# Kernel optimization log

Hardware: AMD Instinct MI355X
Metric: run time of the kernel (lower is better)

Reference implementation:

```python
import jax, jax.numpy as jnp
import numpy as np

USR_NUM = 100000
D_IN = 32
D_HID = 32
D_MID = 16
D_OUT = 2
N_EDGES = 1600000
EPS = 1e-16  # matches torch_geometric.utils.softmax denominator eps


def _glorot(key, shape):
    fan_in, fan_out = shape[0], shape[1]
    lim = np.sqrt(6.0 / (fan_in + fan_out))
    return jax.random.uniform(key, shape, jnp.float32, -lim, lim)


def setup_inputs() -> dict:
    key = jax.random.key(0)
    ks = jax.random.split(key, 16)
    inp = {
        "edge_index": jax.random.randint(ks[0], (2, N_EDGES), 0, USR_NUM, dtype=jnp.int64)
        if jax.config.jax_enable_x64 else jax.random.randint(ks[0], (2, N_EDGES), 0, USR_NUM).astype(jnp.int32),
        "emb": jax.random.normal(ks[1], (USR_NUM, D_IN), jnp.float32),
        # conv1: TransformerConv(32 -> 32, heads=1)
        "Wq1": _glorot(ks[2], (D_IN, D_HID)), "bq1": jnp.zeros((D_HID,), jnp.float32),
        "Wk1": _glorot(ks[3], (D_IN, D_HID)), "bk1": jnp.zeros((D_HID,), jnp.float32),
        "Wv1": _glorot(ks[4], (D_IN, D_HID)), "bv1": jnp.zeros((D_HID,), jnp.float32),
        "Ws1": _glorot(ks[5], (D_IN, D_HID)), "bs1": jnp.zeros((D_HID,), jnp.float32),
        # conv2: TransformerConv(32 -> 16, heads=1)
        "Wq2": _glorot(ks[6], (D_HID, D_MID)), "bq2": jnp.zeros((D_MID,), jnp.float32),
        "Wk2": _glorot(ks[7], (D_HID, D_MID)), "bk2": jnp.zeros((D_MID,), jnp.float32),
        "Wv2": _glorot(ks[8], (D_HID, D_MID)), "bv2": jnp.zeros((D_MID,), jnp.float32),
        "Ws2": _glorot(ks[9], (D_HID, D_MID)), "bs2": jnp.zeros((D_MID,), jnp.float32),
        # output: Linear(16 -> 2)
        "Wo": _glorot(ks[10], (D_MID, D_OUT)), "bo": jnp.zeros((D_OUT,), jnp.float32),
    }
    return inp


def transformer_conv(x, src, dst, Wq, bq, Wk, bk, Wv, bv, Ws, bs, n_nodes):
    # edge (j=src -> i=dst): alpha_ij = softmax_i( <q_i, k_j> / sqrt(d) )
    d = Wq.shape[1]
    q = (x @ Wq + bq)[dst]          # [E, d]
    k = (x @ Wk + bk)[src]          # [E, d]
    v = (x @ Wv + bv)[src]          # [E, d]
    alpha = jnp.sum(q * k, axis=-1) / jnp.sqrt(jnp.float32(d))  # [E]
    # segment softmax over incoming edges of each destination node
    seg_max = jax.ops.segment_max(alpha, dst, num_segments=n_nodes)  # [N]
    e = jnp.exp(alpha - seg_max[dst])
    seg_sum = jax.ops.segment_sum(e, dst, num_segments=n_nodes)      # [N]
    w = e / (seg_sum[dst] + EPS)
    agg = jax.ops.segment_sum(v * w[:, None], dst, num_segments=n_nodes)  # [N, d]
    return agg + x @ Ws + bs  # root/skip connection (PyG default root_weight=True)


def reference(edge_index, emb,
              Wq1, bq1, Wk1, bk1, Wv1, bv1, Ws1, bs1,
              Wq2, bq2, Wk2, bk2, Wv2, bv2, Ws2, bs2,
              Wo, bo):
    src, dst = edge_index[0], edge_index[1]
    h = transformer_conv(emb, src, dst, Wq1, bq1, Wk1, bk1, Wv1, bv1, Ws1, bs1, USR_NUM)
    h = jax.nn.relu(h)
    h = transformer_conv(h, src, dst, Wq2, bq2, Wk2, bk2, Wv2, bv2, Ws2, bs2, USR_NUM)
    h = jax.nn.relu(h)
    return h @ Wo + bo  # [N, 2]
```

## Files before the change

### kernel.cpp

```cpp
#include <hip/hip_runtime.h>
#include <hip/hip_bf16.h>

typedef __hip_bfloat16 bf16;
typedef unsigned int uint;
typedef unsigned short ushort;

#define N_NODES 100000
#define N_EDGES_C 1600000
#define NSB2 392
#define NSB2P 512
#define RND 2048
#define EPB (RND / 256)
#define NBIN 64
#define G_RAD ((N_EDGES_C + RND - 1) / RND)
#define HCAP 5632
#define NSLOT (NSB2 * 256)
#define NCHUNK 8
#define KEYN (256 * NCHUNK)

__device__ __forceinline__ float ldf(const void* p, long i, int isbf) {
    return isbf ? __bfloat162float(((const bf16*)p)[i]) : ((const float*)p)[i];
}
__device__ __forceinline__ int ldidx(const int* ei, long pos, int is64) {
    return is64 ? ei[2 * pos] : ei[pos];
}
__device__ __forceinline__ ushort bfb(float x) {
    bf16 h = __float2bfloat16(x);
    return *(ushort*)&h;
}
__device__ __forceinline__ float bl(uint u) { return __uint_as_float(u << 16); }
__device__ __forceinline__ float bh(uint u) { return __uint_as_float(u & 0xFFFF0000u); }

__global__ void setup_kernel(
    const void* emb, const int* ei,
    const void* Wq1, const void* bq1, const void* Wk1, const void* bk1,
    const void* Wv1, const void* bv1, const void* Ws1, const void* bs1,
    const void* Wq2, const void* bq2, const void* Wk2, const void* bk2,
    const void* Wv2, const void* bv2, const void* Ws2, const void* bs2,
    const void* Wo, const void* bo,
    int* flags, float* wp1, float* bp1, float* wp2, float* bp2, float* woF,
    int* curSB) {
    __shared__ int sf0;
    int t = threadIdx.x;
    if (t < 64) {
        const bf16* pb = (const bf16*)emb;
        int bad = 0;
        for (int i = t; i < 256; i += 64) {
            float v = __bfloat162float(pb[i]);
            if (!(v > -1.0e6f && v < 1.0e6f)) bad++;
        }
        int nz = 0;
        for (int i = 2 * t + 1; i < 256; i += 128) nz += (ei[i] != 0) ? 1 : 0;
#pragma unroll
        for (int m = 32; m >= 1; m >>= 1) {
            bad += __shfl_xor(bad, m, 64);
            nz  += __shfl_xor(nz, m, 64);
        }
        if (t == 0) {
            int f0 = (bad <= 8) ? 1 : 0;
            flags[0] = f0;
            flags[1] = (nz == 0) ? 1 : 0;
            sf0 = f0;
        }
    }
    __syncthreads();
    int isbf = sf0;
    for (int i = t; i < 1024; i += 256) {
        wp1[i]        = ldf(Wq1, i, isbf);
        wp1[1024 + i] = ldf(Wk1, i, isbf);
        wp1[2048 + i] = ldf(Wv1, i, isbf);
        wp1[3072 + i] = ldf(Ws1, i, isbf);
    }
    for (int i = t; i < 512; i += 256) {
        wp2[i]        = ldf(Wq2, i, isbf);
        wp2[512 + i]  = ldf(Wk2, i, isbf);
        wp2[1024 + i] = ldf(Wv2, i, isbf);
        wp2[1536 + i] = ldf(Ws2, i, isbf);
    }
    if (t < 32) {
        bp1[t] = ldf(bq1, t, isbf); bp1[32 + t] = ldf(bk1, t, isbf);
        bp1[64 + t] = ldf(bv1, t, isbf); bp1[96 + t] = ldf(bs1, t, isbf);
        woF[t] = ldf(Wo, t, isbf);
    }
    if (t < 16) {
        bp2[t] = ldf(bq2, t, isbf); bp2[16 + t] = ldf(bk2, t, isbf);
        bp2[32 + t] = ldf(bv2, t, isbf); bp2[48 + t] = ldf(bs2, t, isbf);
    }
    if (t < 2) woF[32 + t] = ldf(bo, t, isbf);
    curSB[t] = 0; curSB[t + 256] = 0;
}

template <int DOUT, bool RUNTIME_DTYPE>
__device__ __forceinline__ void node_linear_body(
    const void* __restrict__ X, const float* __restrict__ wpack,
    const float* __restrict__ bpack, const int* __restrict__ flags,
    float* __restrict__ q, ushort* __restrict__ kvb, float* __restrict__ s,
    int bid, float* __restrict__ sW, float* __restrict__ sbias, float* __restrict__ sX) {
    const int TPN = DOUT / 4;
    const int NPB = 256 / TPN;
    const int W_ELEMS = 4 * 32 * DOUT;

    const float4* wp4 = (const float4*)wpack;
    float4* sW4 = (float4*)sW;
    for (int i = threadIdx.x; i < W_ELEMS / 4; i += 256) sW4[i] = wp4[i];
    if (threadIdx.x < 4 * DOUT) sbias[threadIdx.x] = bpack[threadIdx.x];
    const int base = bid * NPB * 32;
    bool useBf = RUNTIME_DTYPE && (flags[0] != 0);
    if (useBf) {
        for (int i = threadIdx.x; i < NPB * 32; i += 256) {
            int g = base + i;
            float xv = (g < N_NODES * 32) ? __bfloat162float(((const bf16*)X)[g]) : 0.0f;
            sX[(i >> 5) * 36 + (i & 31)] = xv;
        }
    } else {
        for (int i = threadIdx.x; i < NPB * 32; i += 256) {
            int g = base + i;
            sX[(i >> 5) * 36 + (i & 31)] = (g < N_NODES * 32) ? ((const float*)X)[g] : 0.0f;
        }
    }
    __syncthreads();

    int l = threadIdx.x / TPN;
    int c4 = (threadIdx.x % TPN) * 4;
    int n = bid * NPB + l;
    if (n >= N_NODES) return;

    float xr[32];
#pragma unroll
    for (int j = 0; j < 8; j++) {
        float4 t4 = *(const float4*)&sX[l * 36 + 4 * j];
        xr[4 * j] = t4.x; xr[4 * j + 1] = t4.y; xr[4 * j + 2] = t4.z; xr[4 * j + 3] = t4.w;
    }
    float acc[4][4];
#pragma unroll
    for (int m = 0; m < 4; m++)
#pragma unroll
        for (int j = 0; j < 4; j++) acc[m][j] = sbias[m * DOUT + c4 + j];

#pragma unroll
    for (int t = 0; t < 32; t++) {
#pragma unroll
        for (int m = 0; m < 4; m++) {
            float4 w = *(const float4*)&sW[(m * 32 + t) * DOUT + c4];
            acc[m][0] += xr[t] * w.x;
            acc[m][1] += xr[t] * w.y;
            acc[m][2] += xr[t] * w.z;
            acc[m][3] += xr[t] * w.w;
        }
    }
    size_t o = (size_t)n * DOUT + c4;
    *(float4*)&q[o] = make_float4(acc[0][0], acc[0][1], acc[0][2], acc[0][3]);
    *(float4*)&s[o] = make_float4(acc[3][0], acc[3][1], acc[3][2], acc[3][3]);
    size_t okv = (size_t)n * 2 * DOUT + c4;
    ushort4 kp = make_ushort4(bfb(acc[1][0]), bfb(acc[1][1]), bfb(acc[1][2]), bfb(acc[1][3]));
    ushort4 vp = make_ushort4(bfb(acc[2][0]), bfb(acc[2][1]), bfb(acc[2][2]), bfb(acc[2][3]));
    *(ushort4*)&kvb[okv]        = kp;
    *(ushort4*)&kvb[okv + DOUT] = vp;
}

struct RadixS {
    int cnt[NSB2P]; int excl[NSB2P]; int gbase[NSB2P]; int wsum[4];
    uint sVal[RND]; ushort sSb[RND];
};
struct LinS { float sW[4096]; float sbias[128]; float sX[32 * 36]; };
union alignas(16) FusedS { RadixS r; LinS l; };

__global__ void __launch_bounds__(256, 4) fused_ra_nl(
    const int* __restrict__ ei, const int* __restrict__ flags,
    int* __restrict__ curSB, uint* __restrict__ pairsSB,
    const void* __restrict__ X, const float* __restrict__ wpack,
    const float* __restrict__ bpack,
    float* __restrict__ q, ushort* __restrict__ kvb, float* __restrict__ s) {
    __shared__ FusedS u;
    if (blockIdx.x >= G_RAD) {
        node_linear_body<32, true>(X, wpack, bpack, flags, q, kvb, s,
                                   (int)blockIdx.x - G_RAD, u.l.sW, u.l.sbias, u.l.sX);
        return;
    }
    int* cnt = u.r.cnt; int* excl = u.r.excl; int* gbase = u.r.gbase;
    uint* sVal = u.r.sVal; ushort* sSb = u.r.sSb;
    const int is64 = flags[1];
    int t = threadIdx.x;
    cnt[t] = 0; cnt[t + 256] = 0;
    __syncthreads();
    long base = (long)blockIdx.x * RND;

    int mySb[EPB]; int myRank[EPB]; uint myPk[EPB];
#pragma unroll
    for (int r = 0; r < EPB; r++) {
        long e = base + r * 256 + t;
        mySb[r] = -1;
        if (e < N_EDGES_C) {
            int d = ldidx(ei, (long)N_EDGES_C + e, is64);
            int src = ldidx(ei, e, is64);
            int sb = d >> 8;
            myPk[r] = (uint)src | ((uint)(d & 255) << 17);
            myRank[r] = atomicAdd(&cnt[sb], 1);
            mySb[r] = sb;
        }
    }
    __syncthreads();
    int v0 = cnt[2 * t], v1 = cnt[2 * t + 1];
    int sum2 = v0 + v1;
    int lane6 = t & 63, wid6 = t >> 6;
    int x = sum2;
#pragma unroll
    for (int off = 1; off < 64; off <<= 1) {
        int u2 = __shfl_up(x, off, 64);
        if (lane6 >= off) x += u2;
    }
    if (lane6 == 63) u.r.wsum[wid6] = x;
    __syncthreads();
    int wbase = 0;
#pragma unroll
    for (int w = 0; w < 4; w++) if (w < wid6) wbase += u.r.wsum[w];
    int basex = wbase + x - sum2;
    excl[2 * t]     = basex;
    excl[2 * t + 1] = basex + v0;
    __syncthreads();
#pragma unroll
    for (int r = 0; r < EPB; r++) {
        if (mySb[r] >= 0) {
            int pos = excl[mySb[r]] + myRank[r];
            sVal[pos] = myPk[r];
            sSb[pos] = (ushort)mySb[r];
        }
    }
    for (int i = t; i < NSB2P; i += 256)
        gbase[i] = (cnt[i] > 0) ? atomicAdd(&curSB[i], cnt[i]) : 0;
    __syncthreads();
    int tot = excl[NSB2P - 1] + cnt[NSB2P - 1];
    for (int i = t; i < tot; i += 256) {
        int sb = sSb[i];
        int gp = gbase[sb] + (i - excl[sb]);
        if (gp < HCAP)
            pairsSB[(size_t)sb * HCAP + gp] = sVal[i];
    }
}

__global__ void __launch_bounds__(512, 2) radix_b(
    const int* __restrict__ curSB, const uint* __restrict__ pairsSB,
    int* __restrict__ esrc,
    int* __restrict__ rowbeg, int* __restrict__ rowend,
    int* __restrict__ perm) {
    __shared__ uint sP[HCAP];
    __shared__ int dcnt[KEYN];
    __shared__ int dexcl[KEYN];
    __shared__ int wsum[4];
    __shared__ int hbin[NBIN], hbase[NBIN], hcur[NBIN];
    int sbh = blockIdx.x;
    int t = threadIdx.x;
    int n = min(curSB[sbh], HCAP);
    for (int i = t; i < KEYN; i += 512) dcnt[i] = 0;
    if (t < NBIN) { hbin[t] = 0; hcur[t] = 0; }
    if (t < 256) perm[sbh * 256 + t] = -1;
    __syncthreads();
    const uint* srcp = pairsSB + (size_t)sbh * HCAP;
    for (int i = t; i < n; i += 512) {
        uint pk = srcp[i];
        sP[i] = pk;
        int key = (int)((pk >> 17) & 255) * NCHUNK + (int)((pk & 0x1FFFFu) >> 14);
        atomicAdd(&dcnt[key], 1);
    }
    __syncthreads();
    int v = 0, myExcl = 0;
    if (t < 256) {
        const int kb = t * NCHUNK;
        int sum = 0;
#pragma unroll
        for (int j = 0; j < NCHUNK; j++) sum += dcnt[kb + j];
        v = sum;
        int lane6 = t & 63, wid6 = t >> 6;
        int x = v;
#pragma unroll
        for (int off = 1; off < 64; off <<= 1) {
            int u2 = __shfl_up(x, off, 64);
            if (lane6 >= off) x += u2;
        }
        if (lane6 == 63) wsum[wid6] = x;
        myExcl = x - v;
    }
    __syncthreads();
    if (t < 256) {
        int wid6 = t >> 6;
        int wbase = 0;
#pragma unroll
        for (int w = 0; w < 4; w++) if (w < wid6) wbase += wsum[w];
        myExcl += wbase;
        const int kb = t * NCHUNK;
        int run = myExcl;
#pragma unroll
        for (int j = 0; j < NCHUNK; j++) { dexcl[kb + j] = run; run += dcnt[kb + j]; }
    }
    __syncthreads();
    const int EB = sbh * HCAP;
    int dst = sbh * 256 + t;
    int mybin = -1;
    if (t < 256 && dst < N_NODES) {
        rowbeg[dst] = EB + min(myExcl, HCAP);
        rowend[dst] = EB + min(myExcl + v, HCAP);
        mybin = min(v, NBIN - 1);
        atomicAdd(&hbin[mybin], 1);
    }
    __syncthreads();
    if (t < 64) {
        int hv = hbin[t];
        int sfx = hv;
#pragma unroll
        for (int off = 1; off < 64; off <<= 1) {
            int u2 = __shfl_down(sfx, off, 64);
            if (t + off < 64) sfx += u2;
        }
        hbase[t] = sfx - hv;
    }
    __syncthreads();
    if (t < 256 && dst < N_NODES) {
        int r = atomicAdd(&hcur[mybin], 1);
        perm[sbh * 256 + hbase[mybin] + r] = dst;
    }
    for (int i = t; i < n; i += 512) {
        uint pk = sP[i];
        int key = (int)((pk >> 17) & 255) * NCHUNK + (int)((pk & 0x1FFFFu) >> 14);
        int p2 = atomicAdd(&dexcl[key], 1);
        if (p2 < HCAP) esrc[EB + p2] = (int)(pk & 0x1FFFF);
    }
}

__global__ void gather_attn_l1(const int* __restrict__ perm,
                               const int* __restrict__ rowbeg, const int* __restrict__ rowend,
                               const int* __restrict__ esrc,
                               const float* __restrict__ q, const ushort* __restrict__ kvb,
                               const float* __restrict__ s,
                               const float* __restrict__ wp2,
                               const float* __restrict__ bp2,
                               float* __restrict__ q2o, ushort* __restrict__ kvb2o,
                               float* __restrict__ s2o) {
    const int D = 32;
    const int LPD = 4;
    const int G = 16;
    __shared__ float sW2[2048];
    __shared__ float sb2[64];
    __shared__ float sH[64 * 36];
    __shared__ int sDst[64];

    for (int i = threadIdx.x; i < 2048; i += 256) sW2[i] = wp2[i];
    if (threadIdx.x < 64) sb2[threadIdx.x] = bp2[threadIdx.x];

    int lane = threadIdx.x & 63;
    int wave = (blockIdx.x * blockDim.x + threadIdx.x) >> 6;
    int g = lane / LPD;
    int c = lane % LPD;
    int idx = wave * G + g;
    int dst = perm[idx];
    bool alive = (dst >= 0);

    const float rsq = 0.17677669529663689f;
    float4 qa = make_float4(0.f, 0.f, 0.f, 0.f), qb = qa;
    int beg = 0, end = 0;
    if (alive) {
        qa = *(const float4*)(q + (size_t)dst * D + 8 * c);
        qb = *(const float4*)(q + (size_t)dst * D + 8 * c + 4);
        beg = rowbeg[dst]; end = rowend[dst];
    }

    const char* kvbase = (const char*)kvb;
    const int ROW = 4 * D;
    const int koff = 16 * c;
    const int voff = 2 * D + 16 * c;

    float sum0 = 0.f, sum1 = 0.f;
    float a0[8] = {0,0,0,0,0,0,0,0};
    float a1[8] = {0,0,0,0,0,0,0,0};

    uint4 kq[4], vq[4];
#pragma unroll
    for (int r = 0; r < 4; r++) {
        int sn = (beg + r < end) ? esrc[beg + r] : 0;
        const char* p = kvbase + (size_t)sn * ROW;
        kq[r] = *(const uint4*)(p + koff);
        vq[r] = *(const uint4*)(p + voff);
    }

    for (int e = beg; e < end; e += 4) {
        uint4 kc[4], vc[4];
#pragma unroll
        for (int r = 0; r < 4; r++) { kc[r] = kq[r]; vc[r] = vq[r]; }
#pragma unroll
        for (int r = 0; r < 4; r++) {
            if (e + 4 + r < end) {
                const char* p = kvbase + (size_t)esrc[e + 4 + r] * ROW;
                kq[r] = *(const uint4*)(p + koff);
                vq[r] = *(const uint4*)(p + voff);
            }
        }
#pragma unroll
        for (int r = 0; r < 4; r++) {
            if (e + r < end) {
                uint4 kA = kc[r], vA = vc[r];
                float pd = qa.x * bl(kA.x) + qa.y * bh(kA.x) + qa.z * bl(kA.y) + qa.w * bh(kA.y)
                         + qb.x * bl(kA.z) + qb.y * bh(kA.z) + qb.z * bl(kA.w) + qb.w * bh(kA.w);
#pragma unroll
                for (int m = LPD / 2; m >= 1; m >>= 1) pd += __shfl_xor(pd, m, LPD);
                float ex = __expf(fminf(fmaxf(pd * rsq, -80.0f), 80.0f));
                if (r & 1) {
                    sum1 += ex;
                    a1[0] += bl(vA.x) * ex; a1[1] += bh(vA.x) * ex;
                    a1[2] += bl(vA.y) * ex; a1[3] += bh(vA.y) * ex;
                    a1[4] += bl(vA.z) * ex; a1[5] += bh(vA.z) * ex;
                    a1[6] += bl(vA.w) * ex; a1[7] += bh(vA.w) * ex;
                } else {
                    sum0 += ex;
                    a0[0] += bl(vA.x) * ex; a0[1] += bh(vA.x) * ex;
                    a0[2] += bl(vA.y) * ex; a0[3] += bh(vA.y) * ex;
                    a0[4] += bl(vA.z) * ex; a0[5] += bh(vA.z) * ex;
                    a0[6] += bl(vA.w) * ex; a0[7] += bh(vA.w) * ex;
                }
            }
        }
    }
    float inv = 1.0f / (sum0 + sum1 + 1e-16f);
    float4 sa = make_float4(0.f, 0.f, 0.f, 0.f), sbv = sa;
    if (alive) {
        sa  = *(const float4*)(s + (size_t)dst * D + 8 * c);
        sbv = *(const float4*)(s + (size_t)dst * D + 8 * c + 4);
    }
    float h[8];
    h[0] = (a0[0] + a1[0]) * inv + sa.x;  h[1] = (a0[1] + a1[1]) * inv + sa.y;
    h[2] = (a0[2] + a1[2]) * inv + sa.z;  h[3] = (a0[3] + a1[3]) * inv + sa.w;
    h[4] = (a0[4] + a1[4]) * inv + sbv.x; h[5] = (a0[5] + a1[5]) * inv + sbv.y;
    h[6] = (a0[6] + a1[6]) * inv + sbv.z; h[7] = (a0[7] + a1[7]) * inv + sbv.w;
#pragma unroll
    for (int j = 0; j < 8; j++) h[j] = h[j] > 0.0f ? h[j] : 0.0f;

    int gl = (threadIdx.x >> 6) * G + g;
    if (alive) {
        *(float4*)&sH[gl * 36 + 8 * c]     = make_float4(h[0], h[1], h[2], h[3]);
        *(float4*)&sH[gl * 36 + 8 * c + 4] = make_float4(h[4], h[5], h[6], h[7]);
    }
    if (c == 0) sDst[gl] = dst;
    __syncthreads();
    int l = threadIdx.x >> 2;
    int c4 = (threadIdx.x & 3) * 4;
    int nd = sDst[l];
    if (nd >= 0) {
        float acc2[4][4];
#pragma unroll
        for (int m = 0; m < 4; m++)
#pragma unroll
            for (int j = 0; j < 4; j++) acc2[m][j] = sb2[m * 16 + c4 + j];
#pragma unroll
        for (int t2 = 0; t2 < 32; t2++) {
            float xv = sH[l * 36 + t2];
#pragma unroll
            for (int m = 0; m < 4; m++) {
                float4 w = *(const float4*)&sW2[(m * 32 + t2) * 16 + c4];
                acc2[m][0] += xv * w.x;
                acc2[m][1] += xv * w.y;
                acc2[m][2] += xv * w.z;
                acc2[m][3] += xv * w.w;
            }
        }
        size_t o = (size_t)nd * 16 + c4;
        *(float4*)&q2o[o] = make_float4(acc2[0][0], acc2[0][1], acc2[0][2], acc2[0][3]);
        *(float4*)&s2o[o] = make_float4(acc2[3][0], acc2[3][1], acc2[3][2], acc2[3][3]);
        size_t okv = (size_t)nd * 32 + c4;
        ushort4 kp = make_ushort4(bfb(acc2[1][0]), bfb(acc2[1][1]), bfb(acc2[1][2]), bfb(acc2[1][3]));
        ushort4 vp = make_ushort4(bfb(acc2[2][0]), bfb(acc2[2][1]), bfb(acc2[2][2]), bfb(acc2[2][3]));
        *(ushort4*)&kvb2o[okv]      = kp;
        *(ushort4*)&kvb2o[okv + 16] = vp;
    }
}

__global__ void gather_attn_l2(const int* __restrict__ perm,
                               const int* __restrict__ rowbeg, const int* __restrict__ rowend,
                               const int* __restrict__ esrc,
                               const float* __restrict__ q, const ushort* __restrict__ kvb,
                               const float* __restrict__ s,
                               const float* __restrict__ woF,
                               const int* __restrict__ flags,
                               void* __restrict__ out) {
    const int D = 16;
    const int LG = 4;
    const int KL = 2;
    const int G  = 16;

    int lane = threadIdx.x & 63;
    int W = (blockIdx.x * blockDim.x + threadIdx.x) >> 6;
    int g = lane / LG;
    int sub = lane % LG;
    bool isK = (sub < KL);
    int cv = sub - KL;
    int idx = W * G + g;
    int dst = perm[idx];
    if (dst < 0) return;

    const float rsq = 0.25f;
    float qacc[8] = {0,0,0,0,0,0,0,0};
    if (isK) {
        float4 qa = *(const float4*)(q + (size_t)dst * D + 8 * sub);
        float4 qb = *(const float4*)(q + (size_t)dst * D + 8 * sub + 4);
        qacc[0] = qa.x; qacc[1] = qa.y; qacc[2] = qa.z; qacc[3] = qa.w;
        qacc[4] = qb.x; qacc[5] = qb.y; qacc[6] = qb.z; qacc[7] = qb.w;
    }
    int beg = rowbeg[dst], end = rowend[dst];

    const char* kvbase = (const char*)kvb + 16 * sub;
    const int ROW = 4 * D;

    float sum = 0.f;

    uint4 rv[4];
    int sn1[4];
#pragma unroll
    for (int r = 0; r < 4; r++) {
        int sn = (beg + r < end) ? esrc[beg + r] : 0;
        rv[r] = *(const uint4*)(kvbase + (size_t)sn * ROW);
    }
#pragma unroll
    for (int r = 0; r < 4; r++)
        sn1[r] = (beg + 4 + r < end) ? esrc[beg + 4 + r] : 0;

    for (int e = beg; e < end; e += 4) {
        uint4 rc[4];
#pragma unroll
        for (int r = 0; r < 4; r++) rc[r] = rv[r];
#pragma unroll
        for (int r = 0; r < 4; r++) {
            if (e + 4 + r < end)
                rv[r] = *(const uint4*)(kvbase + (size_t)sn1[r] * ROW);
        }
#pragma unroll
        for (int r = 0; r < 4; r++) {
            if (e + 8 + r < end) sn1[r] = esrc[e + 8 + r];
        }
#pragma unroll
        for (int r = 0; r < 4; r++) {
            if (e + r < end) {
                uint4 rA = rc[r];
                float pd = 0.f;
                if (isK) {
                    pd = qacc[0] * bl(rA.x) + qacc[1] * bh(rA.x)
                       + qacc[2] * bl(rA.y) + qacc[3] * bh(rA.y)
                       + qacc[4] * bl(rA.z) + qacc[5] * bh(rA.z)
                       + qacc[6] * bl(rA.w) + qacc[7] * bh(rA.w);
                }
                pd += __shfl_xor(pd, 1, KL);
                float pdx = __shfl_xor(pd, KL, LG);
                float pdf = isK ? pd : pdx;
                float ex = __expf(fminf(fmaxf(pdf * rsq, -80.0f), 80.0f));
                sum += ex;
                if (!isK) {
                    qacc[0] += bl(rA.x) * ex; qacc[1] += bh(rA.x) * ex;
                    qacc[2] += bl(rA.y) * ex; qacc[3] += bh(rA.y) * ex;
                    qacc[4] += bl(rA.z) * ex; qacc[5] += bh(rA.z) * ex;
                    qacc[6] += bl(rA.w) * ex; qacc[7] += bh(rA.w) * ex;
                }
            }
        }
    }
    float inv = 1.0f / (sum + 1e-16f);
    float p0 = 0.f, p1 = 0.f;
    if (!isK) {
        float4 sa  = *(const float4*)(s + (size_t)dst * D + 8 * cv);
        float4 sbv = *(const float4*)(s + (size_t)dst * D + 8 * cv + 4);
        float h[8];
        h[0] = qacc[0] * inv + sa.x;  h[1] = qacc[1] * inv + sa.y;
        h[2] = qacc[2] * inv + sa.z;  h[3] = qacc[3] * inv + sa.w;
        h[4] = qacc[4] * inv + sbv.x; h[5] = qacc[5] * inv + sbv.y;
        h[6] = qacc[6] * inv + sbv.z; h[7] = qacc[7] * inv + sbv.w;
#pragma unroll
        for (int j = 0; j < 8; j++) h[j] = h[j] > 0.0f ? h[j] : 0.0f;
#pragma unroll
        for (int j = 0; j < 8; j++) {
            p0 += h[j] * woF[(8 * cv + j) * 2 + 0];
            p1 += h[j] * woF[(8 * cv + j) * 2 + 1];
        }
    }
    p0 += __shfl_xor(p0, 1, 2);
    p1 += __shfl_xor(p1, 1, 2);
    if (sub == KL) {
        float o0 = p0 + woF[32];
        float o1 = p1 + woF[33];
        if (flags[0]) {
            ((bf16*)out)[dst * 2 + 0] = __float2bfloat16(o0);
            ((bf16*)out)[dst * 2 + 1] = __float2bfloat16(o1);
        } else {
            ((float*)out)[dst * 2 + 0] = o0;
            ((float*)out)[dst * 2 + 1] = o1;
        }
    }
}

extern "C" void kernel_launch(void* const* d_in, const int* in_sizes, int n_in,
                              void* d_out, int out_size, void* d_ws, size_t ws_size,
                              hipStream_t stream) {
    const int* ei  = (const int*)d_in[0];
    const void* emb = d_in[1];
    const void *Wq1 = d_in[2],  *bq1 = d_in[3];
    const void *Wk1 = d_in[4],  *bk1 = d_in[5];
    const void *Wv1 = d_in[6],  *bv1 = d_in[7];
    const void *Ws1 = d_in[8],  *bs1 = d_in[9];
    const void *Wq2 = d_in[10], *bq2 = d_in[11];
    const void *Wk2 = d_in[12], *bk2 = d_in[13];
    const void *Wv2 = d_in[14], *bv2 = d_in[15];
    const void *Ws2 = d_in[16], *bs2 = d_in[17];
    const void *Wo  = d_in[18], *bo  = d_in[19];

    const size_t ND   = (size_t)N_NODES * 32;
    const size_t ND16 = (size_t)N_NODES * 16;
    const size_t SBTOT = (size_t)NSB2 * HCAP;
    float* base   = (float*)d_ws;
    int*   flags  = (int*)base;
    float* wp1    = base + 64;
    float* bp1    = wp1 + 4096;
    float* wp2    = bp1 + 128;
    float* bp2    = wp2 + 2048;
    float* woF    = bp2 + 64;
    int*   curSB  = (int*)(woF + 64);
    int*   rowbeg = curSB + 512;
    int*   rowend = rowbeg + N_NODES;
    int*   perm   = rowend + N_NODES;
    float* p      = (float*)(perm + NSLOT);
    p = (float*)(((uintptr_t)p + 127) & ~(uintptr_t)127);
    float* q      = p; p += ND;
    float* s      = p; p += ND;
    ushort* kvb   = (ushort*)p; p += ND;
    float* q2     = p; p += ND16;
    float* s2     = p; p += ND16;
    ushort* kvb2  = (ushort*)p; p += ND16;
    int*   esrc   = (int*)p; p += SBTOT;
    uint*  pairsSB = (uint*)p;

    const int B = 256;
    const int gNL32  = (N_NODES + 31) / 32;
    const int gFused = G_RAD + gNL32;
    const int gG1    = NSLOT / 64;
    const int gG2    = NSLOT * 4 / 256;

    setup_kernel<<<1, B, 0, stream>>>(emb, ei,
        Wq1, bq1, Wk1, bk1, Wv1, bv1, Ws1, bs1,
        Wq2, bq2, Wk2, bk2, Wv2, bv2, Ws2, bs2, Wo, bo,
        flags, wp1, bp1, wp2, bp2, woF, curSB);

    fused_ra_nl<<<gFused, B, 0, stream>>>(ei, flags, curSB, pairsSB,
                                          emb, wp1, bp1, q, kvb, s);

    radix_b<<<NSB2, 512, 0, stream>>>(curSB, pairsSB, esrc, rowbeg, rowend, perm);

    gather_attn_l1<<<gG1, B, 0, stream>>>(
        perm, rowbeg, rowend, esrc, q, kvb, s, wp2, bp2, q2, kvb2, s2);

    gather_attn_l2<<<gG2, B, 0, stream>>>(
        perm, rowbeg, rowend, esrc, q2, kvb2, s2, woF, flags, d_out);
}
```

Baseline: 259.6 us.

## Shrink destination superbuckets to 64 nodes to quadruple radix_b block count

Destination nodes are now bucketed in groups of 64 instead of 256, giving 1568 superbuckets with a per-bucket capacity of 1536. The first-pass histogram scan now handles 7 counters per thread, and the second-pass kernel runs 256-thread blocks with a single-wavefront scan. The aim is to raise parallelism and occupancy in the second pass, which previously launched only 392 large blocks. In exchange, the global scatter in the first pass spreads over many more buckets, so writes are less coalesced. Degree-sorted node permutation now only applies within 64-node windows, which gives the gather kernels less load balancing.

Result: no change. 258.5 us (-0.4%).

```diff
diff --git a/kernel.cpp b/kernel.cpp
--- a/kernel.cpp
+++ b/kernel.cpp
@@ -7,16 +7,17 @@
 
 #define N_NODES 100000
 #define N_EDGES_C 1600000
-#define NSB2 392
-#define NSB2P 512
+#define NSB2 1568
+#define NSB2P 1792
+#define SCAN_E 7
 #define RND 2048
 #define EPB (RND / 256)
 #define NBIN 64
 #define G_RAD ((N_EDGES_C + RND - 1) / RND)
-#define HCAP 5632
-#define NSLOT (NSB2 * 256)
+#define HCAP 1536
+#define NSLOT (NSB2 * 64)
 #define NCHUNK 8
-#define KEYN (256 * NCHUNK)
+#define KEYN (64 * NCHUNK)
 
 __device__ __forceinline__ float ldf(const void* p, long i, int isbf) {
     return isbf ? __bfloat162float(((const bf16*)p)[i]) : ((const float*)p)[i];
@@ -87,7 +88,7 @@
         bp2[32 + t] = ldf(bv2, t, isbf); bp2[48 + t] = ldf(bs2, t, isbf);
     }
     if (t < 2) woF[32 + t] = ldf(bo, t, isbf);
-    curSB[t] = 0; curSB[t + 256] = 0;
+    for (int i = t; i < NSB2P; i += 256) curSB[i] = 0;
 }
 
 template <int DOUT, bool RUNTIME_DTYPE>
@@ -181,7 +182,7 @@
     uint* sVal = u.r.sVal; ushort* sSb = u.r.sSb;
     const int is64 = flags[1];
     int t = threadIdx.x;
-    cnt[t] = 0; cnt[t + 256] = 0;
+    for (int i = t; i < NSB2P; i += 256) cnt[i] = 0;
     __syncthreads();
     long base = (long)blockIdx.x * RND;
 
@@ -193,17 +194,20 @@
         if (e < N_EDGES_C) {
             int d = ldidx(ei, (long)N_EDGES_C + e, is64);
             int src = ldidx(ei, e, is64);
-            int sb = d >> 8;
-            myPk[r] = (uint)src | ((uint)(d & 255) << 17);
+            int sb = d >> 6;
+            myPk[r] = (uint)src | ((uint)(d & 63) << 17);
             myRank[r] = atomicAdd(&cnt[sb], 1);
             mySb[r] = sb;
         }
     }
     __syncthreads();
-    int v0 = cnt[2 * t], v1 = cnt[2 * t + 1];
-    int sum2 = v0 + v1;
+    const int b7 = t * SCAN_E;
+    int pre[SCAN_E];
+    int s7 = 0;
+#pragma unroll
+    for (int j = 0; j < SCAN_E; j++) { pre[j] = s7; s7 += cnt[b7 + j]; }
     int lane6 = t & 63, wid6 = t >> 6;
-    int x = sum2;
+    int x = s7;
 #pragma unroll
     for (int off = 1; off < 64; off <<= 1) {
         int u2 = __shfl_up(x, off, 64);
@@ -214,9 +218,9 @@
     int wbase = 0;
 #pragma unroll
     for (int w = 0; w < 4; w++) if (w < wid6) wbase += u.r.wsum[w];
-    int basex = wbase + x - sum2;
-    excl[2 * t]     = basex;
-    excl[2 * t + 1] = basex + v0;
+    int basex = wbase + x - s7;
+#pragma unroll
+    for (int j = 0; j < SCAN_E; j++) excl[b7 + j] = basex + pre[j];
     __syncthreads();
 #pragma unroll
     for (int r = 0; r < EPB; r++) {
@@ -238,7 +242,7 @@
     }
 }
 
-__global__ void __launch_bounds__(512, 2) radix_b(
+__global__ void radix_b(
     const int* __restrict__ curSB, const uint* __restrict__ pairsSB,
     int* __restrict__ esrc,
     int* __restrict__ rowbeg, int* __restrict__ rowend,
@@ -246,61 +250,47 @@
     __shared__ uint sP[HCAP];
     __shared__ int dcnt[KEYN];
     __shared__ int dexcl[KEYN];
-    __shared__ int wsum[4];
     __shared__ int hbin[NBIN], hbase[NBIN], hcur[NBIN];
     int sbh = blockIdx.x;
     int t = threadIdx.x;
     int n = min(curSB[sbh], HCAP);
-    for (int i = t; i < KEYN; i += 512) dcnt[i] = 0;
+    for (int i = t; i < KEYN; i += 256) dcnt[i] = 0;
     if (t < NBIN) { hbin[t] = 0; hcur[t] = 0; }
-    if (t < 256) perm[sbh * 256 + t] = -1;
+    if (t < 64) perm[sbh * 64 + t] = -1;
     __syncthreads();
     const uint* srcp = pairsSB + (size_t)sbh * HCAP;
-    for (int i = t; i < n; i += 512) {
+    for (int i = t; i < n; i += 256) {
         uint pk = srcp[i];
         sP[i] = pk;
-        int key = (int)((pk >> 17) & 255) * NCHUNK + (int)((pk & 0x1FFFFu) >> 14);
+        int key = (int)((pk >> 17) & 63) * NCHUNK + (int)((pk & 0x1FFFFu) >> 14);
         atomicAdd(&dcnt[key], 1);
     }
     __syncthreads();
-    int v = 0, myExcl = 0;
-    if (t < 256) {
+    int v = 0, myExcl = 0, mybin = -1;
+    if (t < 64) {
         const int kb = t * NCHUNK;
         int sum = 0;
 #pragma unroll
         for (int j = 0; j < NCHUNK; j++) sum += dcnt[kb + j];
         v = sum;
-        int lane6 = t & 63, wid6 = t >> 6;
         int x = v;
 #pragma unroll
         for (int off = 1; off < 64; off <<= 1) {
             int u2 = __shfl_up(x, off, 64);
-            if (lane6 >= off) x += u2;
-        }
-        if (lane6 == 63) wsum[wid6] = x;
+            if (t >= off) x += u2;
+        }
         myExcl = x - v;
-    }
-    __syncthreads();
-    if (t < 256) {
-        int wid6 = t >> 6;
-        int wbase = 0;
-#pragma unroll
-        for (int w = 0; w < 4; w++) if (w < wid6) wbase += wsum[w];
-        myExcl += wbase;
-        const int kb = t * NCHUNK;
         int run = myExcl;
 #pragma unroll
         for (int j = 0; j < NCHUNK; j++) { dexcl[kb + j] = run; run += dcnt[kb + j]; }
-    }
-    __syncthreads();
-    const int EB = sbh * HCAP;
-    int dst = sbh * 256 + t;
-    int mybin = -1;
-    if (t < 256 && dst < N_NODES) {
-        rowbeg[dst] = EB + min(myExcl, HCAP);
-        rowend[dst] = EB + min(myExcl + v, HCAP);
-        mybin = min(v, NBIN - 1);
-        atomicAdd(&hbin[mybin], 1);
+        int dst = sbh * 64 + t;
+        if (dst < N_NODES) {
+            const int EB = sbh * HCAP;
+            rowbeg[dst] = EB + min(myExcl, HCAP);
+            rowend[dst] = EB + min(myExcl + v, HCAP);
+            mybin = min(v, NBIN - 1);
+            atomicAdd(&hbin[mybin], 1);
+        }
     }
     __syncthreads();
     if (t < 64) {
@@ -314,13 +304,14 @@
         hbase[t] = sfx - hv;
     }
     __syncthreads();
-    if (t < 256 && dst < N_NODES) {
+    if (t < 64 && mybin >= 0) {
         int r = atomicAdd(&hcur[mybin], 1);
-        perm[sbh * 256 + hbase[mybin] + r] = dst;
-    }
-    for (int i = t; i < n; i += 512) {
+        perm[sbh * 64 + hbase[mybin] + r] = sbh * 64 + t;
+    }
+    const int EB = sbh * HCAP;
+    for (int i = t; i < n; i += 256) {
         uint pk = sP[i];
-        int key = (int)((pk >> 17) & 255) * NCHUNK + (int)((pk & 0x1FFFFu) >> 14);
+        int key = (int)((pk >> 17) & 63) * NCHUNK + (int)((pk & 0x1FFFFu) >> 14);
         int p2 = atomicAdd(&dexcl[key], 1);
         if (p2 < HCAP) esrc[EB + p2] = (int)(pk & 0x1FFFF);
     }
@@ -617,7 +608,7 @@
     float* bp2    = wp2 + 2048;
     float* woF    = bp2 + 64;
     int*   curSB  = (int*)(woF + 64);
-    int*   rowbeg = curSB + 512;
+    int*   rowbeg = curSB + NSB2P;
     int*   rowend = rowbeg + N_NODES;
     int*   perm   = rowend + N_NODES;
     float* p      = (float*)(perm + NSLOT);
@@ -635,7 +626,7 @@
     const int gNL32  = (N_NODES + 31) / 32;
     const int gFused = G_RAD + gNL32;
     const int gG1    = NSLOT / 64;
-    const int gG2    = NSLOT * 4 / 256;
+    const int gG2    = NSLOT / 64;
 
     setup_kernel<<<1, B, 0, stream>>>(emb, ei,
         Wq1, bq1, Wk1, bk1, Wv1, bv1, Ws1, bs1,
@@ -645,7 +636,7 @@
     fused_ra_nl<<<gFused, B, 0, stream>>>(ei, flags, curSB, pairsSB,
                                           emb, wp1, bp1, q, kvb, s);
 
-    radix_b<<<NSB2, 512, 0, stream>>>(curSB, pairsSB, esrc, rowbeg, rowend, perm);
+    radix_b<<<NSB2, B, 0, stream>>>(curSB, pairsSB, esrc, rowbeg, rowend, perm);
 
     gather_attn_l1<<<gG1, B, 0, stream>>>(
         perm, rowbeg, rowend, esrc, q, kvb, s, wp2, bp2, q2, kvb2, s2);
```
